# Optimization experiments

Hardware: AMD Instinct MI355X
Metric: run time of the kernel (lower is better)

## Reference

```python
import jax, jax.numpy as jnp
import numpy as np

B, S, D, H = 8, 1500, 1024, 16
HD = D // H
DFF = 4 * D
EPS = 1e-5


def _xavier(key, shape):
    fan_in, fan_out = shape[1], shape[0]
    limit = float(np.sqrt(6.0 / (fan_in + fan_out)))
    return jax.random.uniform(key, shape, jnp.float32, -limit, limit)


def setup_inputs() -> dict:
    key = jax.random.key(0)
    ks = jax.random.split(key, 8)
    return {
        "hidden_states": jax.random.normal(ks[0], (B, S, D), jnp.float32),
        "Wq": _xavier(ks[1], (D, D)),
        "Wk": _xavier(ks[2], (D, D)),
        "Wv": _xavier(ks[3], (D, D)),
        "Wo": _xavier(ks[4], (D, D)),
        "W1": _xavier(ks[5], (DFF, D)),
        "b1": jnp.zeros((DFF,), jnp.float32),
        "W2": _xavier(ks[6], (D, DFF)),
        "b2": jnp.zeros((D,), jnp.float32),
        "ln1_g": jnp.ones((D,), jnp.float32),
        "ln1_b": jnp.zeros((D,), jnp.float32),
        "ln2_g": jnp.ones((D,), jnp.float32),
        "ln2_b": jnp.zeros((D,), jnp.float32),
    }


def _layernorm(x, g, b):
    mu = jnp.mean(x, axis=-1, keepdims=True)
    var = jnp.mean(jnp.square(x - mu), axis=-1, keepdims=True)
    return (x - mu) * jax.lax.rsqrt(var + EPS) * g + b


def reference(hidden_states, Wq, Wk, Wv, Wo, W1, b1, W2, b2, ln1_g, ln1_b, ln2_g, ln2_b):
    x = hidden_states
    residual = x
    h = _layernorm(x, ln1_g, ln1_b)
    # torch Linear: y = h @ W.T ; reshape to heads
    q = (h @ Wq.T).reshape(B, S, H, HD).transpose(0, 2, 1, 3) * (HD ** -0.5)
    k = (h @ Wk.T).reshape(B, S, H, HD).transpose(0, 2, 1, 3)
    v = (h @ Wv.T).reshape(B, S, H, HD).transpose(0, 2, 1, 3)
    scores = jnp.einsum('bhqd,bhkd->bhqk', q, k)
    attn = jax.nn.softmax(scores.astype(jnp.float32), axis=-1).astype(h.dtype)
    ctx = jnp.einsum('bhqk,bhkd->bhqd', attn, v)
    ctx = ctx.transpose(0, 2, 1, 3).reshape(B, S, D)
    x = residual + ctx @ Wo.T
    residual = x
    h = _layernorm(x, ln2_g, ln2_b)
    ffn = jax.nn.gelu(h @ W1.T + b1, approximate=False) @ W2.T + b2
    return residual + ffn
```

## Files before the change

### kernel.cpp

```cpp
#include <hip/hip_runtime.h>
#include <hip/hip_bf16.h>
#include <cstdint>
#include <cstddef>

#define B_    8
#define S_    1500
#define D_    1024
#define H_    16
#define HD_   64
#define DFF_  4096
#define M_    12000
#define VTS_  1536

typedef __bf16 bf16;
typedef __attribute__((ext_vector_type(8))) __bf16 bf16x8;
typedef __attribute__((ext_vector_type(4))) float f32x4;

#define MFMA16(a, b, c) __builtin_amdgcn_mfma_f32_16x16x32_bf16((a), (b), (c), 0, 0, 0)

#define BAR()   do { __builtin_amdgcn_s_barrier(); __builtin_amdgcn_sched_barrier(0); } while (0)
#define LGKM0() do { asm volatile("s_waitcnt lgkmcnt(0)" ::: "memory"); __builtin_amdgcn_sched_barrier(0); } while (0)

static __device__ __forceinline__ void gload16(const void* g, void* l) {
  __builtin_amdgcn_global_load_lds(
      (const __attribute__((address_space(1))) void*)(uintptr_t)g,
      (__attribute__((address_space(3))) void*)(uintptr_t)l, 16, 0, 0);
}

static __device__ __forceinline__ unsigned short f2bu(float v) {
  bf16 h = (bf16)v;
  union { bf16 h; unsigned short u; } c;
  c.h = h;
  return c.u;
}

static constexpr size_t HSZ      = (size_t)M_ * D_ * 2;
static constexpr size_t H_OFF    = 0;
static constexpr size_t WQ_OFF   = H_OFF + HSZ;
static constexpr size_t WK_OFF   = WQ_OFF + (size_t)D_ * D_ * 2;
static constexpr size_t WV_OFF   = WK_OFF + (size_t)D_ * D_ * 2;
static constexpr size_t WO_OFF   = WV_OFF + (size_t)D_ * D_ * 2;
static constexpr size_t Q_OFF    = WO_OFF + (size_t)D_ * D_ * 2;
static constexpr size_t K_OFF    = Q_OFF + HSZ;
static constexpr size_t VT_OFF   = K_OFF + HSZ;
static constexpr size_t W1_OFF   = VT_OFF + (size_t)128 * 64 * VTS_ * 2;
static constexpr size_t W2_OFF   = W1_OFF + (size_t)DFF_ * D_ * 2;
static constexpr size_t WS_BASE  = W2_OFF + (size_t)DFF_ * D_ * 2;
static constexpr size_t H2B_OFF  = WS_BASE;
static constexpr size_t NEED_BIG = WS_BASE + HSZ;
static constexpr size_t H2F_OFF  = VT_OFF;
static constexpr size_t ACT_OFF  = 0;

__launch_bounds__(256)
__global__ void cvt_bf16(const float* __restrict__ src, bf16* __restrict__ dst, int n) {
  int i = (blockIdx.x * 256 + threadIdx.x) * 4;
  if (i < n) {
    float4 f = *(const float4*)(src + i);
    dst[i + 0] = (bf16)f.x;
    dst[i + 1] = (bf16)f.y;
    dst[i + 2] = (bf16)f.z;
    dst[i + 3] = (bf16)f.w;
  }
}

__launch_bounds__(256)
__global__ void ln_fused(const float* __restrict__ x, const float* __restrict__ g,
                         const float* __restrict__ bb, bf16* __restrict__ out) {
  const int row = blockIdx.x;
  const int t = threadIdx.x;
  const float4 xv = *(const float4*)(x + (size_t)row * D_ + t * 4);
  float s  = xv.x + xv.y + xv.z + xv.w;
  float s2 = xv.x * xv.x + xv.y * xv.y + xv.z * xv.z + xv.w * xv.w;
#pragma unroll
  for (int m = 32; m >= 1; m >>= 1) {
    s  += __shfl_xor(s, m);
    s2 += __shfl_xor(s2, m);
  }
  __shared__ float red[8];
  const int w = t >> 6;
  if ((t & 63) == 0) { red[w] = s; red[4 + w] = s2; }
  __syncthreads();
  s  = red[0] + red[1] + red[2] + red[3];
  s2 = red[4] + red[5] + red[6] + red[7];
  const float mu  = s * (1.0f / D_);
  const float var = s2 * (1.0f / D_) - mu * mu;
  const float rs  = rsqrtf(var + 1e-5f);
  const float4 gv = *(const float4*)(g + t * 4);
  const float4 bv = *(const float4*)(bb + t * 4);
  bf16* o = out + (size_t)row * D_ + t * 4;
  o[0] = (bf16)((xv.x - mu) * rs * gv.x + bv.x);
  o[1] = (bf16)((xv.y - mu) * rs * gv.y + bv.y);
  o[2] = (bf16)((xv.z - mu) * rs * gv.z + bv.z);
  o[3] = (bf16)((xv.w - mu) * rs * gv.w + bv.w);
}

template <int EPI>
__launch_bounds__(512, 2)
__global__ void gemm256(const bf16* __restrict__ A, const bf16* __restrict__ Bw,
                        int M, int N, int K,
                        bf16* __restrict__ outB, float* outF,
                        const float* __restrict__ bias, const float* resid,
                        bf16* __restrict__ outQ, bf16* __restrict__ outK2,
                        bf16* __restrict__ outV) {
  __shared__ bf16 a_lds[4][256 * 32];
  __shared__ bf16 b_lds[4][256 * 32];

  const int t = threadIdx.x;
  const int lane = t & 63, wid = t >> 6;
  const int wm = wid >> 2, wn = wid & 3;
  const int l15 = lane & 15, hi = lane >> 4;
  const int mrow0 = blockIdx.x * 256;
  const int ncol0 = blockIdx.y * 256;

  const int pc = hi ^ ((l15 >> 1) & 3);

  const int s0 = t, s1 = 512 + t;
  const int ar0 = s0 >> 2, ar1 = s1 >> 2;
  const int ac0 = ((s0 & 3) ^ ((ar0 >> 1) & 3)) * 8;
  const int ac1 = ((s1 & 3) ^ ((ar1 >> 1) & 3)) * 8;
  int ga0 = mrow0 + ar0; ga0 = ga0 < M ? ga0 : M - 1;
  int ga1 = mrow0 + ar1; ga1 = ga1 < M ? ga1 : M - 1;
  const bf16* a0 = A + (size_t)ga0 * K + ac0;
  const bf16* a1 = A + (size_t)ga1 * K + ac1;
  const bf16* b0 = Bw + (size_t)(ncol0 + ar0) * K + ac0;
  const bf16* b1 = Bw + (size_t)(ncol0 + ar1) * K + ac1;

  f32x4 acc[8][4] = {};

  const int NT = K >> 5;

  gload16(a0,      (char*)&a_lds[0][0] + s0 * 16);
  gload16(a1,      (char*)&a_lds[0][0] + s1 * 16);
  gload16(b0,      (char*)&b_lds[0][0] + s0 * 16);
  gload16(b1,      (char*)&b_lds[0][0] + s1 * 16);
  gload16(a0 + 32, (char*)&a_lds[1][0] + s0 * 16);
  gload16(a1 + 32, (char*)&a_lds[1][0] + s1 * 16);
  gload16(b0 + 32, (char*)&b_lds[1][0] + s0 * 16);
  gload16(b1 + 32, (char*)&b_lds[1][0] + s1 * 16);
  asm volatile("s_waitcnt vmcnt(4)" ::: "memory");
  BAR();

  int buf = 0;
  for (int tt = 0; tt < NT; ++tt) {
    const bf16* al = &a_lds[buf][0];
    const bf16* bl = &b_lds[buf][0];
    const bool do_stage = (tt + 2) < NT;
    const int nb = (tt + 2) & 3;
    const int k2 = (tt + 2) << 5;

    if (do_stage) {
      gload16(a0 + k2, (char*)&a_lds[nb][0] + s0 * 16);
      gload16(a1 + k2, (char*)&a_lds[nb][0] + s1 * 16);
    }
    bf16x8 bf_[4], af_[4];
#pragma unroll
    for (int n = 0; n < 4; ++n)
      bf_[n] = *(const bf16x8*)&bl[(wn * 64 + n * 16 + l15) * 32 + pc * 8];
#pragma unroll
    for (int m = 0; m < 4; ++m)
      af_[m] = *(const bf16x8*)&al[(wm * 128 + m * 16 + l15) * 32 + pc * 8];
    BAR();
    LGKM0();
    __builtin_amdgcn_s_setprio(1);
#pragma unroll
    for (int m = 0; m < 4; ++m)
#pragma unroll
      for (int n = 0; n < 4; ++n)
        acc[m][n] = MFMA16(af_[m], bf_[n], acc[m][n]);
    __builtin_amdgcn_s_setprio(0);
    BAR();

    if (do_stage) {
      gload16(b0 + k2, (char*)&b_lds[nb][0] + s0 * 16);
      gload16(b1 + k2, (char*)&b_lds[nb][0] + s1 * 16);
    }
#pragma unroll
    for (int m = 0; m < 4; ++m)
      af_[m] = *(const bf16x8*)&al[(wm * 128 + (m + 4) * 16 + l15) * 32 + pc * 8];
    BAR();
    LGKM0();
    __builtin_amdgcn_s_setprio(1);
#pragma unroll
    for (int m = 0; m < 4; ++m)
#pragma unroll
      for (int n = 0; n < 4; ++n)
        acc[m + 4][n] = MFMA16(af_[m], bf_[n], acc[m + 4][n]);
    __builtin_amdgcn_s_setprio(0);
    if (do_stage) asm volatile("s_waitcnt vmcnt(4)" ::: "memory");
    else          asm volatile("s_waitcnt vmcnt(0)" ::: "memory");
    BAR();
    buf = (buf + 1) & 3;
  }

  const int r0 = hi * 4;

  if constexpr (EPI == 5) {
    const int mm = blockIdx.y >> 2;
    const int nloc0 = (blockIdx.y & 3) * 256;
    if (mm == 2) {
#pragma unroll
      for (int m = 0; m < 8; ++m) {
        int row0 = mrow0 + wm * 128 + m * 16 + r0;
        if (row0 < M) {
          int bb2 = row0 / 1500;
          int s = row0 - bb2 * 1500;
#pragma unroll
          for (int n = 0; n < 4; ++n) {
            int f = nloc0 + wn * 64 + n * 16 + l15;
            size_t a = ((size_t)(bb2 * 16 + (f >> 6)) * 64 + (f & 63)) * VTS_ + s;
            ushort4 pk;
            pk.x = f2bu(acc[m][n][0]);
            pk.y = f2bu(acc[m][n][1]);
            pk.z = f2bu(acc[m][n][2]);
            pk.w = f2bu(acc[m][n][3]);
            *reinterpret_cast<ushort4*>((unsigned short*)outV + a) = pk;
          }
        }
      }
    } else {
      bf16* dst = (mm == 0) ? outQ : outK2;
      const float sc = (mm == 0) ? 0.18033688011112042f : 1.0f;
#pragma unroll
      for (int m = 0; m < 8; ++m) {
#pragma unroll
        for (int n = 0; n < 4; ++n) {
          int col = nloc0 + wn * 64 + n * 16 + l15;
#pragma unroll
          for (int r = 0; r < 4; ++r) {
            int row = mrow0 + wm * 128 + m * 16 + r0 + r;
            if (row < M) dst[(size_t)row * D_ + col] = (bf16)(acc[m][n][r] * sc);
          }
        }
      }
    }
    return;
  }

#pragma unroll
  for (int m = 0; m < 8; ++m) {
#pragma unroll
    for (int n = 0; n < 4; ++n) {
      int col = ncol0 + wn * 64 + n * 16 + l15;
#pragma unroll
      for (int r = 0; r < 4; ++r) {
        int row = mrow0 + wm * 128 + m * 16 + r0 + r;
        if (row < M) {
          float v = acc[m][n][r];
          if constexpr (EPI == 2) {
            float xg = v + bias[col];
            v = 0.5f * xg * (1.0f + erff(xg * 0.70710678118654752f));
            outB[(size_t)row * N + col] = (bf16)v;
          }
          if constexpr (EPI == 3) {
            v += resid[(size_t)row * N + col];
            if (bias) v += bias[col];
            outF[(size_t)row * N + col] = v;
          }
        }
      }
    }
  }
}

template <int EPI>
__launch_bounds__(256)
__global__ void gemm_bt(const bf16* __restrict__ A, const bf16* __restrict__ Bw,
                        int M, int N, int K,
                        bf16* __restrict__ outB, float* outF,
                        const float* __restrict__ bias, const float* resid,
                        float scale) {
  __shared__ bf16 a_lds[128 * 64];
  __shared__ bf16 b_lds[128 * 64];
  const int t = threadIdx.x;
  const int lane = t & 63, wid = t >> 6;
  const int wr = wid >> 1, wc = wid & 1;
  const int mrow0 = blockIdx.x * 128;
  const int ncol0 = blockIdx.y * 128;
  const int l15 = lane & 15;
  const int khi = (lane >> 4) << 3;

  f32x4 acc[4][4] = {};

  for (int k0 = 0; k0 < K; k0 += 64) {
#pragma unroll
    for (int i = 0; i < 4; ++i) {
      int idx = i * 2048 + t * 8;
      int row = idx >> 6, col = idx & 63;
      int gr = mrow0 + row;
      gr = gr < M ? gr : M - 1;
      gload16(A + (size_t)gr * K + (k0 + col), (char*)a_lds + idx * 2);
    }
#pragma unroll
    for (int i = 0; i < 4; ++i) {
      int idx = i * 2048 + t * 8;
      int row = idx >> 6, col = idx & 63;
      gload16(Bw + (size_t)(ncol0 + row) * K + (k0 + col), (char*)b_lds + idx * 2);
    }
    __syncthreads();
#pragma unroll
    for (int kk = 0; kk < 2; ++kk) {
      bf16x8 af[4], bfv[4];
#pragma unroll
      for (int m = 0; m < 4; ++m)
        af[m] = *(const bf16x8*)&a_lds[(wr * 64 + m * 16 + l15) * 64 + kk * 32 + khi];
#pragma unroll
      for (int n = 0; n < 4; ++n)
        bfv[n] = *(const bf16x8*)&b_lds[(wc * 64 + n * 16 + l15) * 64 + kk * 32 + khi];
#pragma unroll
      for (int m = 0; m < 4; ++m)
#pragma unroll
        for (int n = 0; n < 4; ++n)
          acc[m][n] = MFMA16(af[m], bfv[n], acc[m][n]);
    }
    __syncthreads();
  }

  const int r0 = (lane >> 4) << 2;
#pragma unroll
  for (int m = 0; m < 4; ++m) {
#pragma unroll
    for (int n = 0; n < 4; ++n) {
      int col = ncol0 + wc * 64 + n * 16 + l15;
#pragma unroll
      for (int r = 0; r < 4; ++r) {
        int row = mrow0 + wr * 64 + m * 16 + r0 + r;
        if (row < M) {
          float v = acc[m][n][r];
          if constexpr (EPI == 2) {
            float xg = v + bias[col];
            v = 0.5f * xg * (1.0f + erff(xg * 0.70710678118654752f));
          }
          if constexpr (EPI == 3) {
            v += resid[(size_t)row * N + col];
            if (bias) v += bias[col];
            outF[(size_t)row * N + col] = v;
          } else {
            outB[(size_t)row * N + col] = (bf16)v;
          }
        }
      }
    }
  }
}

__launch_bounds__(256, 4)
__global__ void attn_fwd6(const bf16* __restrict__ q, const bf16* __restrict__ kg,
                          const bf16* __restrict__ vt, bf16* __restrict__ cx) {
  __shared__ bf16 k_lds[2][64 * 64];
  __shared__ bf16 v_lds[2][64 * 64];
  __shared__ bf16 p_lds[4][16 * 64];

  const int t = threadIdx.x;
  const int lane = t & 63, w = t >> 6;
  const int L = blockIdx.x;
  const int wu = (L & 7) * 384 + (L >> 3);
  const int bh = wu / 24;
  const int qt = wu - bh * 24;
  const int l15 = lane & 15;
  const int hi = lane >> 4;
  const int khi = hi << 3;

  const size_t hoff = ((size_t)(bh >> 4) * S_) * D_ + (size_t)(bh & 15) * HD_;
  const bf16* qh = q + hoff;
  const bf16* kh = kg + hoff;
  const bf16* vh = vt + (size_t)bh * (64 * VTS_);

  const int st_r0 = t >> 3;
  const int st_c  = t & 7;

  int qr = qt * 64 + w * 16 + l15;
  int qrc = qr < S_ ? qr : S_ - 1;
  const bf16x8 qf0 = *(const bf16x8*)(qh + (size_t)qrc * D_ + khi);
  const bf16x8 qf1 = *(const bf16x8*)(qh + (size_t)qrc * D_ + 32 + khi);

  f32x4 oacc[4] = {};
  float mrun[4], lrun[4];
#pragma unroll
  for (int r = 0; r < 4; ++r) { mrun[r] = -1e30f; lrun[r] = 0.f; }

  bf16* pw = &p_lds[w][0];
  const int NT = (S_ + 63) / 64;
  const float THR = 11.5415605f;

#pragma unroll
  for (int i = 0; i < 2; ++i) {
    int row = i * 32 + st_r0;
    int sc = st_c ^ (row & 7);
    int key = row < S_ ? row : S_ - 1;
    gload16(kh + (size_t)key * D_ + sc * 8, (char*)&k_lds[0][0] + (i * 2048 + t * 8) * 2);
    gload16(vh + (size_t)row * VTS_ + sc * 8, (char*)&v_lds[0][0] + (i * 2048 + t * 8) * 2);
  }
  __syncthreads();

  int buf = 0;
  for (int kt = 0; kt < NT; ++kt) {
    if (kt + 1 < NT) {
      int kb = (kt + 1) * 64;
#pragma unroll
      for (int i = 0; i < 2; ++i) {
        int row = i * 32 + st_r0;
        int sc = st_c ^ (row & 7);
        int key = kb + row;
        key = key < S_ ? key : S_ - 1;
        gload16(kh + (size_t)key * D_ + sc * 8,
                (char*)&k_lds[buf ^ 1][0] + (i * 2048 + t * 8) * 2);
        gload16(vh + (size_t)row * VTS_ + kb + sc * 8,
                (char*)&v_lds[buf ^ 1][0] + (i * 2048 + t * 8) * 2);
      }
    }

    float pv[4][4];
    __builtin_amdgcn_s_setprio(1);
#pragma unroll
    for (int nb = 0; nb < 4; ++nb) {
      int krow = nb * 16 + l15;
      f32x4 z = {};
      z = MFMA16(qf0, *(const bf16x8*)&k_lds[buf][krow * 64 + ((hi ^ (l15 & 7)) << 3)], z);
      z = MFMA16(qf1, *(const bf16x8*)&k_lds[buf][krow * 64 + (((4 + hi) ^ (l15 & 7)) << 3)], z);
#pragma unroll
      for (int r = 0; r < 4; ++r) pv[nb][r] = z[r];
    }
    __builtin_amdgcn_s_setprio(0);

    if (kt == NT - 1) {
#pragma unroll
      for (int nb = 0; nb < 4; ++nb) {
        bool cvld = (kt * 64 + nb * 16 + l15) < S_;
#pragma unroll
        for (int r = 0; r < 4; ++r) pv[nb][r] = cvld ? pv[nb][r] : -1e30f;
      }
    }

    float lmax[4];
    bool ok = true;
#pragma unroll
    for (int r = 0; r < 4; ++r) {
      lmax[r] = fmaxf(fmaxf(pv[0][r], pv[1][r]), fmaxf(pv[2][r], pv[3][r]));
      ok = ok && (lmax[r] <= mrun[r] + THR);
    }
    if (!__all(ok)) {
#pragma unroll
      for (int r = 0; r < 4; ++r) {
        float mx = lmax[r];
        mx = fmaxf(mx, __shfl_xor(mx, 1));
        mx = fmaxf(mx, __shfl_xor(mx, 2));
        mx = fmaxf(mx, __shfl_xor(mx, 4));
        mx = fmaxf(mx, __shfl_xor(mx, 8));
        float mnew = fmaxf(mrun[r], mx);
        float corr = exp2f(mrun[r] - mnew);
        lrun[r] *= corr;
        mrun[r] = mnew;
#pragma unroll
        for (int db = 0; db < 4; ++db) oacc[db][r] *= corr;
      }
    }

#pragma unroll
    for (int r = 0; r < 4; ++r) {
      float p0 = exp2f(pv[0][r] - mrun[r]);
      float p1 = exp2f(pv[1][r] - mrun[r]);
      float p2 = exp2f(pv[2][r] - mrun[r]);
      float p3 = exp2f(pv[3][r] - mrun[r]);
      pv[0][r] = p0; pv[1][r] = p1; pv[2][r] = p2; pv[3][r] = p3;
      lrun[r] += (p0 + p1) + (p2 + p3);
    }

#pragma unroll
    for (int nb = 0; nb < 4; ++nb) {
#pragma unroll
      for (int r = 0; r < 4; ++r) {
        int prow = hi * 4 + r;
        int pcol = (nb * 16 + l15) ^ ((prow & 7) << 3);
        pw[prow * 64 + pcol] = (bf16)pv[nb][r];
      }
    }

    __builtin_amdgcn_s_setprio(1);
#pragma unroll
    for (int kk = 0; kk < 2; ++kk) {
      bf16x8 pf = *(const bf16x8*)&pw[l15 * 64 + (((kk * 4 + hi) ^ (l15 & 7)) << 3)];
#pragma unroll
      for (int db = 0; db < 4; ++db) {
        int vrow = db * 16 + l15;
        bf16x8 vf = *(const bf16x8*)&v_lds[buf][vrow * 64 + (((kk * 4 + hi) ^ (l15 & 7)) << 3)];
        oacc[db] = MFMA16(pf, vf, oacc[db]);
      }
    }
    __builtin_amdgcn_s_setprio(0);

    __syncthreads();
    buf ^= 1;
  }

#pragma unroll
  for (int r = 0; r < 4; ++r) {
    float ps = lrun[r];
    ps += __shfl_xor(ps, 1);
    ps += __shfl_xor(ps, 2);
    ps += __shfl_xor(ps, 4);
    ps += __shfl_xor(ps, 8);
    int qrow = qt * 64 + w * 16 + hi * 4 + r;
    if (qrow < S_) {
      float inv = 1.0f / ps;
#pragma unroll
      for (int db = 0; db < 4; ++db)
        cx[hoff + (size_t)qrow * D_ + db * 16 + l15] = (bf16)(oacc[db][r] * inv);
    }
  }
}

extern "C" void kernel_launch(void* const* d_in, const int* in_sizes, int n_in,
                              void* d_out, int out_size, void* d_ws, size_t ws_size,
                              hipStream_t stream) {
  const float* x   = (const float*)d_in[0];
  const float* Wq  = (const float*)d_in[1];
  const float* Wk  = (const float*)d_in[2];
  const float* Wv  = (const float*)d_in[3];
  const float* Wo  = (const float*)d_in[4];
  const float* W1  = (const float*)d_in[5];
  const float* b1  = (const float*)d_in[6];
  const float* W2  = (const float*)d_in[7];
  const float* b2  = (const float*)d_in[8];
  const float* g1  = (const float*)d_in[9];
  const float* be1 = (const float*)d_in[10];
  const float* g2  = (const float*)d_in[11];
  const float* be2 = (const float*)d_in[12];
  float* out = (float*)d_out;

  char* ws = (char*)d_ws;
  bf16* h_b   = (bf16*)(ws + H_OFF);
  bf16* wq_b  = (bf16*)(ws + WQ_OFF);
  bf16* wk_b  = (bf16*)(ws + WK_OFF);
  bf16* wv_b  = (bf16*)(ws + WV_OFF);
  bf16* wo_b  = (bf16*)(ws + WO_OFF);
  bf16* w1_b  = (bf16*)(ws + W1_OFF);
  bf16* w2_b  = (bf16*)(ws + W2_OFF);
  bf16* q_b   = (bf16*)(ws + Q_OFF);
  bf16* k_b   = (bf16*)(ws + K_OFF);
  bf16* vt_b  = (bf16*)(ws + VT_OFF);
  bf16* act_b = (bf16*)(ws + ACT_OFF);
  bf16* ctx_b = h_b;

  const bool big = ws_size >= NEED_BIG;
  bf16* h2_b = (bf16*)(ws + (big ? H2B_OFF : H2F_OFF));

  cvt_bf16<<<(D_ * D_) / 1024, 256, 0, stream>>>(Wq, wq_b, D_ * D_);
  cvt_bf16<<<(D_ * D_) / 1024, 256, 0, stream>>>(Wk, wk_b, D_ * D_);
  cvt_bf16<<<(D_ * D_) / 1024, 256, 0, stream>>>(Wv, wv_b, D_ * D_);
  cvt_bf16<<<(D_ * D_) / 1024, 256, 0, stream>>>(Wo, wo_b, D_ * D_);
  cvt_bf16<<<(DFF_ * D_) / 1024, 256, 0, stream>>>(W1, w1_b, DFF_ * D_);
  cvt_bf16<<<(DFF_ * D_) / 1024, 256, 0, stream>>>(W2, w2_b, DFF_ * D_);

  ln_fused<<<M_, 256, 0, stream>>>(x, g1, be1, h_b);

  gemm256<5><<<dim3((M_ + 255) / 256, 12), 512, 0, stream>>>(
      h_b, wq_b, M_, 3072, D_, nullptr, nullptr, nullptr, nullptr, q_b, k_b, vt_b);

  attn_fwd6<<<3072, 256, 0, stream>>>(q_b, k_b, vt_b, ctx_b);

  gemm256<3><<<dim3((M_ + 255) / 256, 4), 512, 0, stream>>>(
      ctx_b, wo_b, M_, D_, D_, nullptr, out, nullptr, x, nullptr, nullptr, nullptr);

  ln_fused<<<M_, 256, 0, stream>>>(out, g2, be2, h2_b);

  if (big) {
    gemm256<2><<<dim3((M_ + 255) / 256, DFF_ / 256), 512, 0, stream>>>(
        h2_b, w1_b, M_, DFF_, D_, act_b, nullptr, b1, nullptr,
        nullptr, nullptr, nullptr);
    gemm256<3><<<dim3((M_ + 255) / 256, D_ / 256), 512, 0, stream>>>(
        act_b, w2_b, M_, D_, DFF_, nullptr, out, b2, out,
        nullptr, nullptr, nullptr);
  } else {
    for (int c = 0; c < 3; ++c) {
      int r0c = c * 4000;
      int nr = 4000;
      gemm256<2><<<dim3((nr + 255) / 256, DFF_ / 256), 512, 0, stream>>>(
          h2_b + (size_t)r0c * D_, w1_b, nr, DFF_, D_, act_b, nullptr, b1, nullptr,
          nullptr, nullptr, nullptr);
      gemm_bt<3><<<dim3((nr + 127) / 128, D_ / 128), 256, 0, stream>>>(
          act_b, w2_b, nr, D_, DFF_, nullptr, out + (size_t)r0c * D_, b2,
          out + (size_t)r0c * D_, 0.f);
    }
  }
}
```

Before: 733.1 us.

## Restructure GEMM main loop to K=64 tiles with double-buffered quadrant schedule

The 256x256 GEMM main loop now uses K-tiles of 64 with two LDS buffers instead of four 32-wide buffers. Each iteration is split into four MFMA quadrant phases, with the next tile's A and B row-groups staged between phases and a new XOR swizzle over 8 column chunks. The aim is to halve the number of outer iterations and barriers per unit of K and to interleave global-to-LDS loads with compute more finely. In exchange there are more barriers per iteration, and the prefetch distance drops to one tile, which could expose load latency.

New measurement: 721.5 us. No clear change (-1.6%).

```diff
diff --git a/kernel.cpp b/kernel.cpp
--- a/kernel.cpp
+++ b/kernel.cpp
@@ -20,6 +20,7 @@
 
 #define BAR()   do { __builtin_amdgcn_s_barrier(); __builtin_amdgcn_sched_barrier(0); } while (0)
 #define LGKM0() do { asm volatile("s_waitcnt lgkmcnt(0)" ::: "memory"); __builtin_amdgcn_sched_barrier(0); } while (0)
+#define VMCNT(n) asm volatile("s_waitcnt vmcnt(" #n ")" ::: "memory")
 
 static __device__ __forceinline__ void gload16(const void* g, void* l) {
   __builtin_amdgcn_global_load_lds(
@@ -102,8 +103,8 @@
                         const float* __restrict__ bias, const float* resid,
                         bf16* __restrict__ outQ, bf16* __restrict__ outK2,
                         bf16* __restrict__ outV) {
-  __shared__ bf16 a_lds[4][256 * 32];
-  __shared__ bf16 b_lds[4][256 * 32];
+  __shared__ bf16 a_lds[2][256 * 64];
+  __shared__ bf16 b_lds[2][256 * 64];
 
   const int t = threadIdx.x;
   const int lane = t & 63, wid = t >> 6;
@@ -111,85 +112,137 @@
   const int l15 = lane & 15, hi = lane >> 4;
   const int mrow0 = blockIdx.x * 256;
   const int ncol0 = blockIdx.y * 256;
-
-  const int pc = hi ^ ((l15 >> 1) & 3);
-
-  const int s0 = t, s1 = 512 + t;
-  const int ar0 = s0 >> 2, ar1 = s1 >> 2;
-  const int ac0 = ((s0 & 3) ^ ((ar0 >> 1) & 3)) * 8;
-  const int ac1 = ((s1 & 3) ^ ((ar1 >> 1) & 3)) * 8;
-  int ga0 = mrow0 + ar0; ga0 = ga0 < M ? ga0 : M - 1;
-  int ga1 = mrow0 + ar1; ga1 = ga1 < M ? ga1 : M - 1;
-  const bf16* a0 = A + (size_t)ga0 * K + ac0;
-  const bf16* a1 = A + (size_t)ga1 * K + ac1;
-  const bf16* b0 = Bw + (size_t)(ncol0 + ar0) * K + ac0;
-  const bf16* b1 = Bw + (size_t)(ncol0 + ar1) * K + ac1;
+  const int l7 = l15 & 7;
+
+  const int rl = t >> 3;
+  const int sc8 = ((t & 7) ^ (rl & 7)) << 3;
+  unsigned offA[4], offB[4];
+#pragma unroll
+  for (int r = 0; r < 4; ++r) {
+    int gr = mrow0 + r * 64 + rl; gr = gr < M ? gr : M - 1;
+    offA[r] = (unsigned)gr * (unsigned)K + (unsigned)sc8;
+    offB[r] = (unsigned)(ncol0 + r * 64 + rl) * (unsigned)K + (unsigned)sc8;
+  }
 
   f32x4 acc[8][4] = {};
-
-  const int NT = K >> 5;
-
-  gload16(a0,      (char*)&a_lds[0][0] + s0 * 16);
-  gload16(a1,      (char*)&a_lds[0][0] + s1 * 16);
-  gload16(b0,      (char*)&b_lds[0][0] + s0 * 16);
-  gload16(b1,      (char*)&b_lds[0][0] + s1 * 16);
-  gload16(a0 + 32, (char*)&a_lds[1][0] + s0 * 16);
-  gload16(a1 + 32, (char*)&a_lds[1][0] + s1 * 16);
-  gload16(b0 + 32, (char*)&b_lds[1][0] + s0 * 16);
-  gload16(b1 + 32, (char*)&b_lds[1][0] + s1 * 16);
-  asm volatile("s_waitcnt vmcnt(4)" ::: "memory");
+  bf16x8 afA[4][2], bfB[4][2];
+
+  const int NT = K >> 6;
+
+  {
+    char* ad = (char*)&a_lds[0][0];
+    char* bd = (char*)&b_lds[0][0];
+    gload16(A + offA[0], ad + t * 16);
+    gload16(A + offA[2], ad + 16384 + t * 16);
+    gload16(Bw + offB[0], bd + t * 16);
+    gload16(Bw + offB[1], bd + 8192 + t * 16);
+    gload16(Bw + offB[2], bd + 16384 + t * 16);
+    gload16(Bw + offB[3], bd + 24576 + t * 16);
+    gload16(A + offA[1], ad + 8192 + t * 16);
+    gload16(A + offA[3], ad + 24576 + t * 16);
+  }
+  VMCNT(2);
   BAR();
 
-  int buf = 0;
-  for (int tt = 0; tt < NT; ++tt) {
-    const bf16* al = &a_lds[buf][0];
-    const bf16* bl = &b_lds[buf][0];
-    const bool do_stage = (tt + 2) < NT;
-    const int nb = (tt + 2) & 3;
-    const int k2 = (tt + 2) << 5;
-
-    if (do_stage) {
-      gload16(a0 + k2, (char*)&a_lds[nb][0] + s0 * 16);
-      gload16(a1 + k2, (char*)&a_lds[nb][0] + s1 * 16);
-    }
-    bf16x8 bf_[4], af_[4];
-#pragma unroll
-    for (int n = 0; n < 4; ++n)
-      bf_[n] = *(const bf16x8*)&bl[(wn * 64 + n * 16 + l15) * 32 + pc * 8];
+  for (int T = 0; T < NT; ++T) {
+    const bf16* al = &a_lds[T & 1][0];
+    const bf16* bl = &b_lds[T & 1][0];
+    char* ad = (char*)&a_lds[(T + 1) & 1][0];
+    char* bd = (char*)&b_lds[(T + 1) & 1][0];
+    const bool st = (T + 1) < NT;
+    const unsigned k1 = (unsigned)(T + 1) << 6;
+
 #pragma unroll
     for (int m = 0; m < 4; ++m)
-      af_[m] = *(const bf16x8*)&al[(wm * 128 + m * 16 + l15) * 32 + pc * 8];
+#pragma unroll
+      for (int kk = 0; kk < 2; ++kk)
+        afA[m][kk] = *(const bf16x8*)&al[(wm * 128 + m * 16 + l15) * 64 + (((kk * 4 + hi) ^ l7) << 3)];
+#pragma unroll
+    for (int n = 0; n < 2; ++n)
+#pragma unroll
+      for (int kk = 0; kk < 2; ++kk)
+        bfB[n][kk] = *(const bf16x8*)&bl[(wn * 64 + n * 16 + l15) * 64 + (((kk * 4 + hi) ^ l7) << 3)];
+    if (st) {
+      gload16(A + offA[0] + k1, ad + t * 16);
+      gload16(A + offA[2] + k1, ad + 16384 + t * 16);
+    }
     BAR();
     LGKM0();
     __builtin_amdgcn_s_setprio(1);
 #pragma unroll
     for (int m = 0; m < 4; ++m)
 #pragma unroll
-      for (int n = 0; n < 4; ++n)
-        acc[m][n] = MFMA16(af_[m], bf_[n], acc[m][n]);
+      for (int n = 0; n < 2; ++n)
+#pragma unroll
+        for (int kk = 0; kk < 2; ++kk)
+          acc[m][n] = MFMA16(afA[m][kk], bfB[n][kk], acc[m][n]);
     __builtin_amdgcn_s_setprio(0);
     BAR();
 
-    if (do_stage) {
-      gload16(b0 + k2, (char*)&b_lds[nb][0] + s0 * 16);
-      gload16(b1 + k2, (char*)&b_lds[nb][0] + s1 * 16);
-    }
-#pragma unroll
-    for (int m = 0; m < 4; ++m)
-      af_[m] = *(const bf16x8*)&al[(wm * 128 + (m + 4) * 16 + l15) * 32 + pc * 8];
+#pragma unroll
+    for (int n = 2; n < 4; ++n)
+#pragma unroll
+      for (int kk = 0; kk < 2; ++kk)
+        bfB[n][kk] = *(const bf16x8*)&bl[(wn * 64 + n * 16 + l15) * 64 + (((kk * 4 + hi) ^ l7) << 3)];
+    if (st) {
+      gload16(Bw + offB[0] + k1, bd + t * 16);
+      gload16(Bw + offB[1] + k1, bd + 8192 + t * 16);
+      VMCNT(4);
+    } else {
+      VMCNT(0);
+    }
     BAR();
     LGKM0();
     __builtin_amdgcn_s_setprio(1);
 #pragma unroll
     for (int m = 0; m < 4; ++m)
 #pragma unroll
-      for (int n = 0; n < 4; ++n)
-        acc[m + 4][n] = MFMA16(af_[m], bf_[n], acc[m + 4][n]);
+      for (int n = 2; n < 4; ++n)
+#pragma unroll
+        for (int kk = 0; kk < 2; ++kk)
+          acc[m][n] = MFMA16(afA[m][kk], bfB[n][kk], acc[m][n]);
     __builtin_amdgcn_s_setprio(0);
-    if (do_stage) asm volatile("s_waitcnt vmcnt(4)" ::: "memory");
-    else          asm volatile("s_waitcnt vmcnt(0)" ::: "memory");
-    BAR();
-    buf = (buf + 1) & 3;
+    BAR();
+
+#pragma unroll
+    for (int m = 0; m < 4; ++m)
+#pragma unroll
+      for (int kk = 0; kk < 2; ++kk)
+        afA[m][kk] = *(const bf16x8*)&al[(wm * 128 + (m + 4) * 16 + l15) * 64 + (((kk * 4 + hi) ^ l7) << 3)];
+    if (st) {
+      gload16(Bw + offB[2] + k1, bd + 16384 + t * 16);
+      gload16(Bw + offB[3] + k1, bd + 24576 + t * 16);
+    }
+    BAR();
+    LGKM0();
+    __builtin_amdgcn_s_setprio(1);
+#pragma unroll
+    for (int m = 0; m < 4; ++m)
+#pragma unroll
+      for (int n = 0; n < 2; ++n)
+#pragma unroll
+        for (int kk = 0; kk < 2; ++kk)
+          acc[m + 4][n] = MFMA16(afA[m][kk], bfB[n][kk], acc[m + 4][n]);
+    __builtin_amdgcn_s_setprio(0);
+    BAR();
+
+    if (st) {
+      gload16(A + offA[1] + k1, ad + 8192 + t * 16);
+      gload16(A + offA[3] + k1, ad + 24576 + t * 16);
+      VMCNT(2);
+    }
+    BAR();
+    LGKM0();
+    __builtin_amdgcn_s_setprio(1);
+#pragma unroll
+    for (int m = 0; m < 4; ++m)
+#pragma unroll
+      for (int n = 2; n < 4; ++n)
+#pragma unroll
+        for (int kk = 0; kk < 2; ++kk)
+          acc[m + 4][n] = MFMA16(afA[m][kk], bfB[n][kk], acc[m + 4][n]);
+    __builtin_amdgcn_s_setprio(0);
+    BAR();
   }
 
   const int r0 = hi * 4;
```
